# Optimization experiments

Measured on AMD Instinct MI355X. Metric: run time of the kernel, lower is better.

## Reference

```python
import jax, jax.numpy as jnp
import numpy as np

EPS = 1e-08


def setup_inputs() -> dict:
    key = jax.random.key(0)
    k1, k2 = jax.random.split(key)
    query_features = jax.random.normal(k1, (64, 1024, 32, 32), dtype=jnp.float32)
    support_features = jax.random.normal(k2, (25, 1024, 32, 32), dtype=jnp.float32)
    return {"query_features": query_features, "support_features": support_features}


def reference(query_features, support_features):
    B, C, h, w = support_features.shape
    NQ = query_features.shape[0]
    # Covariance over channels: flatten support to (C, B*h*w), center, GEMM.
    support = jnp.transpose(support_features, (1, 0, 2, 3)).reshape(C, -1)
    centered = support - jnp.mean(support, axis=1, keepdims=True)
    N = B * h * w
    cov = (centered @ centered.T) / (N - 1 + EPS)  # (C, C)
    # Queries: (NQ, C, d), L2-normalize each channel row over spatial dim.
    q = query_features.reshape(NQ, C, -1)
    q = q / (jnp.linalg.norm(q, axis=2, keepdims=True) + EPS)
    # diag(q^T cov q) without materializing (d, d): cov@q then elementwise reduce over C.
    cq = jnp.einsum('cD,nDd->ncd', cov, q)  # (NQ, C, d)
    scores = jnp.mean(jnp.sum(q * cq, axis=1), axis=1)  # (NQ,)
    return scores
```

## Files before the change

### kernel.cpp

```cpp
#include <hip/hip_runtime.h>

#define NQ   64
#define CCH  1024
#define DSP  1024
#define NSUP 25600
#define NKT  400
#define NCOVB 252

typedef __attribute__((ext_vector_type(4))) float f32x4;
typedef __attribute__((ext_vector_type(8))) __bf16 bf16x8;

#define WAITVM(N) asm volatile("s_waitcnt vmcnt(" #N ")" ::: "memory")
#define WAITLGKM0() asm volatile("s_waitcnt lgkmcnt(0)" ::: "memory")
#define BAR() __builtin_amdgcn_s_barrier()
#define SCHED0() __builtin_amdgcn_sched_barrier(0)

__device__ inline unsigned short f2bf(float x) {
  unsigned u = __builtin_bit_cast(unsigned, x);
  u += 0x7fffu + ((u >> 16) & 1u);
  return (unsigned short)(u >> 16);
}

__global__ __launch_bounds__(640) void mean_center_kernel(
    const float* __restrict__ sup, float* __restrict__ mean,
    unsigned short* __restrict__ Sb, int write_sb,
    float4* __restrict__ cov4, float4* __restrict__ out4) {
  __shared__ float wred[10];
  __shared__ float mbc;
  const int c = blockIdx.x;
  const int tid = threadIdx.x;
  const int l = tid & 63, wid = tid >> 6;
  const float4 z4 = make_float4(0.f, 0.f, 0.f, 0.f);
  if (tid < 256) cov4[c * 256 + tid] = z4;
  if (c == 0 && tid >= 256 && tid < 272) out4[tid - 256] = z4;

  float4 v[10];
  float s = 0.f;
#pragma unroll
  for (int i = 0; i < 10; ++i) {
    const int qd = i * 640 + tid;
    const int b = qd >> 8, s4 = (qd & 255) << 2;
    v[i] = *(const float4*)(sup + ((size_t)b * CCH + c) * DSP + s4);
    s += v[i].x + v[i].y + v[i].z + v[i].w;
  }
#pragma unroll
  for (int off = 32; off > 0; off >>= 1) s += __shfl_xor(s, off);
  if (l == 0) wred[wid] = s;
  __syncthreads();
  if (tid == 0) {
    float t = 0.f;
#pragma unroll
    for (int i = 0; i < 10; ++i) t += wred[i];
    mbc = t * (1.0f / 25600.0f);
  }
  __syncthreads();
  const float m = mbc;
  if (tid == 0) mean[c] = m;
  if (write_sb) {
#pragma unroll
    for (int i = 0; i < 10; ++i) {
      const int qd = i * 640 + tid;
      const int b = qd >> 8, s4 = (qd & 255) << 2;
      ushort4 o;
      o.x = f2bf(v[i].x - m); o.y = f2bf(v[i].y - m);
      o.z = f2bf(v[i].z - m); o.w = f2bf(v[i].w - m);
      *(ushort4*)(Sb + (size_t)c * NSUP + b * DSP + s4) = o;
    }
  }
}

__global__ __launch_bounds__(256) void qnorm_kernel(
    const float* __restrict__ q, float* __restrict__ qfac,
    unsigned short* __restrict__ Qb, int write_qb) {
  const int row = blockIdx.x * 4 + (threadIdx.x >> 6);
  const int l = threadIdx.x & 63;
  const float4* src = (const float4*)(q + (size_t)row * DSP);
  float4 v[4];
  float ss = 0.f;
#pragma unroll
  for (int i = 0; i < 4; ++i) {
    v[i] = src[l + 64 * i];
    ss += v[i].x * v[i].x + v[i].y * v[i].y + v[i].z * v[i].z + v[i].w * v[i].w;
  }
#pragma unroll
  for (int off = 32; off > 0; off >>= 1) ss += __shfl_xor(ss, off);
  const float f = 1.0f / (sqrtf(ss) + 1e-8f);
  if (l == 0) qfac[row] = f;
  if (write_qb) {
#pragma unroll
    for (int i = 0; i < 4; ++i) {
      ushort4 o;
      o.x = f2bf(v[i].x * f); o.y = f2bf(v[i].y * f);
      o.z = f2bf(v[i].z * f); o.w = f2bf(v[i].w * f);
      *(ushort4*)(Qb + (size_t)row * DSP + (size_t)(l + 64 * i) * 4) = o;
    }
  }
}


__device__ inline void rd4(const unsigned short* base, int r0, int col, int lr, bf16x8 f[4]) {
#pragma unroll
  for (int i = 0; i < 4; ++i)
    f[i] = *(const bf16x8*)(const void*)(base + (r0 + i * 16 + lr) * 64 + col);
}
__device__ inline void mfma16(const bf16x8 a[4], const bf16x8 b[4], f32x4 (*acc)[4]) {
#pragma unroll
  for (int i = 0; i < 4; ++i)
#pragma unroll
    for (int j = 0; j < 4; ++j)
      acc[i][j] = __builtin_amdgcn_mfma_f32_16x16x32_bf16(a[i], b[j], acc[i][j], 0, 0, 0);
}

__device__ inline void stage_glds(const unsigned short* __restrict__ src, int ld,
                                  int row0, int k0, unsigned short* lds) {
  const int tid = threadIdx.x;
  const int w = tid >> 6;
#pragma unroll
  for (int it = 0; it < 4; ++it) {
    const int ci = it * 256 + tid;
    const int r = ci >> 3;
    const int kc = ((ci & 7) ^ (r & 7)) << 3;
    const unsigned short* g = src + (size_t)(row0 + r) * ld + k0 + kc;
    unsigned short* lb = lds + ((it * 256 + w * 64) << 3);
    __builtin_amdgcn_global_load_lds((const __attribute__((address_space(1))) void*)g,
                                     (__attribute__((address_space(3))) void*)lb,
                                     16, 0, 0);
  }
}

__device__ inline void stage256g(const unsigned short* __restrict__ src, int ld,
                                 int row0, int k0, unsigned short* lds_base) {
  const int tid = threadIdx.x;
  const int wid = tid >> 6;
#pragma unroll
  for (int it = 0; it < 4; ++it) {
    const int ci = it * 512 + tid;
    const int r = ci >> 3;
    const int kc = ((ci & 7) ^ (r & 7)) << 3;
    const unsigned short* g = src + (size_t)(row0 + r) * ld + k0 + kc;
    unsigned short* lb = lds_base + ((it * 512 + (wid << 6)) << 3);
    __builtin_amdgcn_global_load_lds((const __attribute__((address_space(1))) void*)g,
                                     (__attribute__((address_space(3))) void*)lb,
                                     16, 0, 0);
  }
}

template <int NT>
__device__ inline void loop256(const unsigned short* __restrict__ src, int ld,
                               int rowA, int rowB, int k0, bool diag,
                               unsigned short* lds,
                               int wm, int wn, int lr, int kg, int sw,
                               f32x4 (*acc)[4]) {
  stage256g(src, ld, rowA, k0, lds);
  if (!diag) stage256g(src, ld, rowB, k0, lds + 16384);
  stage256g(src, ld, rowA, k0 + 64, lds + 32768);
  if (!diag) stage256g(src, ld, rowB, k0 + 64, lds + 32768 + 16384);

  for (int t = 0; t < NT; ++t) {
    const int cb = (t & 1) << 15;
    if (t < NT - 1) { if (diag) { WAITVM(4); } else { WAITVM(8); } }
    else { WAITVM(0); }
    BAR(); SCHED0();
    const unsigned short* A = lds + cb + wm * 8192;
    const unsigned short* B = lds + cb + (diag ? 0 : 16384) + (wn >> 1) * 8192;
    const int brow = (wn & 1) * 64;
    bf16x8 a[4], b[4];
    {
      const int col = kg ^ sw;
      rd4(B, brow, col, lr, b);
      rd4(A, 0, col, lr, a);
      mfma16(a, b, &acc[0]);
      rd4(A, 64, col, lr, a);
      mfma16(a, b, &acc[4]);
    }
    {
      const int col = (32 + kg) ^ sw;
      rd4(B, brow, col, lr, b);
      rd4(A, 0, col, lr, a);
      mfma16(a, b, &acc[0]);
      rd4(A, 64, col, lr, a);
      WAITLGKM0();
      BAR(); SCHED0();
      if (t + 2 < NT) {
        stage256g(src, ld, rowA, k0 + (t + 2) * 64, lds + cb);
        if (!diag) stage256g(src, ld, rowB, k0 + (t + 2) * 64, lds + cb + 16384);
      }
      mfma16(a, b, &acc[4]);
    }
  }
}

__device__ inline void decode_tile8(int t, int& ti, int& tj) {
  int rem = t; ti = 0;
  while (rem >= 8 - ti) { rem -= 8 - ti; ++ti; }
  tj = ti + rem;
}
__device__ inline void decode_pair4(int p, int& ti, int& tj) {
  int rem = p; ti = 0;
  while (rem >= 4 - ti) { rem -= 4 - ti; ++ti; }
  tj = ti + rem;
}

__global__ __launch_bounds__(256) void covq_kernel(
    const unsigned short* __restrict__ Sb, float* __restrict__ cov,
    const float* __restrict__ q, float* __restrict__ qfac,
    unsigned short* __restrict__ Qb) {
  __shared__ unsigned short clds[32768];
  const int bx = blockIdx.x;
  if (bx < NCOVB) {
    const int ks = bx % 7;
    int ti, tj; decode_tile8(bx / 7, ti, tj);
    const bool diag = (ti == tj);
    const int tid = threadIdx.x, l = tid & 63, w = tid >> 6;
    const int wr = (w >> 1) * 64, wc = (w & 1) * 64, lr = l & 15, kg = (l >> 4) * 8;
    const int sw = (lr & 7) << 3;
    f32x4 acc[4][4];
#pragma unroll
    for (int i = 0; i < 4; ++i)
#pragma unroll
      for (int j = 0; j < 4; ++j) acc[i][j] = 0.f;

    const int kt0 = (NKT * ks) / 7;
    const int nt = (NKT * (ks + 1)) / 7 - kt0;
    const int kbase = kt0 * 64;

    stage_glds(Sb, NSUP, ti * 128, kbase, clds);
    if (!diag) stage_glds(Sb, NSUP, tj * 128, kbase, clds + 8192);
    stage_glds(Sb, NSUP, ti * 128, kbase + 64, clds + 16384);
    if (!diag) stage_glds(Sb, NSUP, tj * 128, kbase + 64, clds + 16384 + 8192);
    for (int t = 0; t < nt; ++t) {
      const int cb = (t & 1) * 16384;
      if (t < nt - 1) { if (diag) { WAITVM(4); } else { WAITVM(8); } }
      else { WAITVM(0); }
      BAR(); SCHED0();
      const unsigned short* A = clds + cb;
      const unsigned short* B = diag ? A : A + 8192;
      const int col0 = kg ^ sw, col1 = (32 + kg) ^ sw;
      bf16x8 a[4], b[4];
      rd4(A, wr, col0, lr, a);
      rd4(B, wc, col0, lr, b);
      mfma16(a, b, (f32x4(*)[4])acc);
      rd4(A, wr, col1, lr, a);
      rd4(B, wc, col1, lr, b);
      WAITLGKM0();
      BAR(); SCHED0();
      if (t + 2 < nt) {
        const int k2 = kbase + (t + 2) * 64;
        stage_glds(Sb, NSUP, ti * 128, k2, clds + cb);
        if (!diag) stage_glds(Sb, NSUP, tj * 128, k2, clds + cb + 8192);
      }
      mfma16(a, b, (f32x4(*)[4])acc);
    }

    const float scale = 1.0f / (25599.0f + 1e-8f);
    const int rbase = ti * 128 + wr + (l >> 4) * 4;
    const int cbase = tj * 128 + wc + (l & 15);
#pragma unroll
    for (int i = 0; i < 4; ++i)
#pragma unroll
      for (int j = 0; j < 4; ++j)
#pragma unroll
        for (int r = 0; r < 4; ++r)
          atomicAdd(&cov[(size_t)(rbase + i * 16 + r) * CCH + cbase + j * 16],
                    acc[i][j][r] * scale);
  } else {
    const int row = (bx - NCOVB) * 4 + (threadIdx.x >> 6);
    const int l = threadIdx.x & 63;
    const float4* src = (const float4*)(q + (size_t)row * DSP);
    float4 v[4];
    float ss = 0.f;
#pragma unroll
    for (int i = 0; i < 4; ++i) {
      v[i] = src[l + 64 * i];
      ss += v[i].x * v[i].x + v[i].y * v[i].y + v[i].z * v[i].z + v[i].w * v[i].w;
    }
#pragma unroll
    for (int off = 32; off > 0; off >>= 1) ss += __shfl_xor(ss, off);
    const float f = 1.0f / (sqrtf(ss) + 1e-8f);
    if (l == 0) qfac[row] = f;
#pragma unroll
    for (int i = 0; i < 4; ++i) {
      ushort4 o;
      o.x = f2bf(v[i].x * f); o.y = f2bf(v[i].y * f);
      o.z = f2bf(v[i].z * f); o.w = f2bf(v[i].w * f);
      *(ushort4*)(Qb + (size_t)row * DSP + (size_t)(l + 64 * i) * 4) = o;
    }
  }
}

__global__ __launch_bounds__(512, 2) void gram256_kernel(
    const unsigned short* __restrict__ Qb, const float* __restrict__ cov,
    float* __restrict__ out) {
  __shared__ unsigned short lds[65536];
  const int wg = blockIdx.x;
  const int xcd = wg & 7, slot = wg >> 3;
  const int n = xcd * 8 + slot / 20;
  const int sub = slot % 20;
  const int kh = sub & 1;
  int ti, tj; decode_pair4(sub >> 1, ti, tj);
  const bool diag = (ti == tj);
  const int tid = threadIdx.x, l = tid & 63, wid = tid >> 6;
  const int wm = wid >> 2, wn = wid & 3;
  const int lr = l & 15, kg = (l >> 4) * 8;
  const int sw = (lr & 7) << 3;
  const unsigned short* Qn = Qb + (size_t)n * CCH * DSP;

  f32x4 acc[8][4];
#pragma unroll
  for (int i = 0; i < 8; ++i)
#pragma unroll
    for (int j = 0; j < 4; ++j) acc[i][j] = 0.f;

  loop256<8>(Qn, DSP, ti * 256, tj * 256, kh * 512, diag, lds,
             wm, wn, lr, kg, sw, acc);

  float wgt;
  if (!diag) wgt = 2.0f;
  else if (wm == 0 && (wn >> 1) == 1) wgt = 2.0f;
  else if (wm == 1 && (wn >> 1) == 0) wgt = 0.0f;
  else wgt = 1.0f;

  float s = 0.f;
  if (wgt != 0.0f) {
    const int rbase = ti * 256 + wm * 128 + (l >> 4) * 4;
    const int cbase = tj * 256 + wn * 64 + (l & 15);
#pragma unroll
    for (int i = 0; i < 8; ++i)
#pragma unroll
      for (int j = 0; j < 4; ++j)
#pragma unroll
        for (int r = 0; r < 4; ++r)
          s += acc[i][j][r] * cov[(size_t)(rbase + i * 16 + r) * CCH + cbase + j * 16];
  }
  s *= wgt * (1.0f / 1024.0f);
#pragma unroll
  for (int off = 32; off > 0; off >>= 1) s += __shfl_xor(s, off);
  if (l == 0) atomicAdd(&out[n], s);
}

__device__ inline void mfma16s(const bf16x8 a[4], const bf16x8 b[4], f32x4 acc[4][4]) {
#pragma unroll
  for (int i = 0; i < 4; ++i)
#pragma unroll
    for (int j = 0; j < 4; ++j)
      acc[i][j] = __builtin_amdgcn_mfma_f32_16x16x32_bf16(a[i], b[j], acc[i][j], 0, 0, 0);
}

__device__ inline void stage_sup_f32(const float* __restrict__ sup,
                                     const float* __restrict__ mean,
                                     int row0, int k0, unsigned short* lds) {
  const int tid = threadIdx.x;
#pragma unroll
  for (int it = 0; it < 4; ++it) {
    const int ci = it * 256 + tid;
    const int r = ci >> 3, kc = (ci & 7) << 3;
    const int c = row0 + r;
    const int k = k0 + kc;
    const int b = k >> 10, sp = k & 1023;
    const float4* gp = (const float4*)(sup + ((size_t)b * CCH + c) * DSP + sp);
    const float4 v0 = gp[0], v1 = gp[1];
    const float m = mean[c];
    union { unsigned short h[8]; int4 q; } pk;
    pk.h[0] = f2bf(v0.x - m); pk.h[1] = f2bf(v0.y - m);
    pk.h[2] = f2bf(v0.z - m); pk.h[3] = f2bf(v0.w - m);
    pk.h[4] = f2bf(v1.x - m); pk.h[5] = f2bf(v1.y - m);
    pk.h[6] = f2bf(v1.z - m); pk.h[7] = f2bf(v1.w - m);
    *(int4*)(lds + (size_t)(r * 8 + ((ci & 7) ^ (r & 7))) * 8) = pk.q;
  }
}
__device__ inline void stage_q_f32(const float* __restrict__ qn,
                                   const float* __restrict__ qfacn,
                                   int row0, int k0, unsigned short* lds) {
  const int tid = threadIdx.x;
#pragma unroll
  for (int it = 0; it < 4; ++it) {
    const int ci = it * 256 + tid;
    const int r = ci >> 3, kc = (ci & 7) << 3;
    const int c = row0 + r;
    const float4* gp = (const float4*)(qn + (size_t)c * DSP + k0 + kc);
    const float4 v0 = gp[0], v1 = gp[1];
    const float f = qfacn[c];
    union { unsigned short h[8]; int4 q; } pk;
    pk.h[0] = f2bf(v0.x * f); pk.h[1] = f2bf(v0.y * f);
    pk.h[2] = f2bf(v0.z * f); pk.h[3] = f2bf(v0.w * f);
    pk.h[4] = f2bf(v1.x * f); pk.h[5] = f2bf(v1.y * f);
    pk.h[6] = f2bf(v1.z * f); pk.h[7] = f2bf(v1.w * f);
    *(int4*)(lds + (size_t)(r * 8 + ((ci & 7) ^ (r & 7))) * 8) = pk.q;
  }
}
__device__ inline void compute_step(const unsigned short* lA, const unsigned short* lB,
                                    int wr, int wc, int lr, int kg, f32x4 acc[4][4]) {
  const int sc = (lr & 7) << 3;
#pragma unroll
  for (int kk = 0; kk < 64; kk += 32) {
    const int col = (kk + kg) ^ sc;
    bf16x8 a[4], b[4];
    rd4(lA, wr, col, lr, a);
    rd4(lB, wc, col, lr, b);
    mfma16s(a, b, acc);
  }
}

__global__ __launch_bounds__(256) void cov_kernel_f32(
    const float* __restrict__ sup, const float* __restrict__ mean,
    float* __restrict__ cov) {
  __shared__ unsigned short clds[32768];
  const int wg = blockIdx.x;
  const int ks = wg & 7;
  int ti, tj; decode_tile8(wg >> 3, ti, tj);
  const bool diag = (ti == tj);
  const int tid = threadIdx.x, l = tid & 63, w = tid >> 6;
  const int wr = (w >> 1) * 64, wc = (w & 1) * 64, lr = l & 15, kg = (l >> 4) * 8;
  f32x4 acc[4][4];
#pragma unroll
  for (int i = 0; i < 4; ++i)
#pragma unroll
    for (int j = 0; j < 4; ++j) acc[i][j] = 0.f;

  const int kbase = ks * (NSUP / 8);
  stage_sup_f32(sup, mean, ti * 128, kbase, clds);
  if (!diag) stage_sup_f32(sup, mean, tj * 128, kbase, clds + 8192);
  __syncthreads();
  for (int kt = 0; kt < 50; ++kt) {
    const int cb = (kt & 1) * 16384;
    const int nb = cb ^ 16384;
    if (kt + 1 < 50) {
      const int k1 = kbase + (kt + 1) * 64;
      stage_sup_f32(sup, mean, ti * 128, k1, clds + nb);
      if (!diag) stage_sup_f32(sup, mean, tj * 128, k1, clds + nb + 8192);
    }
    compute_step(clds + cb, diag ? clds + cb : clds + cb + 8192, wr, wc, lr, kg, acc);
    __syncthreads();
  }
  const float scale = 1.0f / (25599.0f + 1e-8f);
  const int rbase = ti * 128 + wr + (l >> 4) * 4;
  const int cbase = tj * 128 + wc + (l & 15);
#pragma unroll
  for (int i = 0; i < 4; ++i)
#pragma unroll
    for (int j = 0; j < 4; ++j)
#pragma unroll
      for (int r = 0; r < 4; ++r)
        atomicAdd(&cov[(size_t)(rbase + i * 16 + r) * CCH + cbase + j * 16],
                  acc[i][j][r] * scale);
}

__global__ __launch_bounds__(256) void gram_kernel_f32(
    const float* __restrict__ q, const float* __restrict__ qfac,
    const float* __restrict__ cov, float* __restrict__ out) {
  __shared__ unsigned short lA[2][128 * 64];
  __shared__ unsigned short lB[2][128 * 64];
  const int wg = blockIdx.x;
  const int xcd = wg & 7, slot = wg >> 3;
  const int n = xcd * 8 + slot / 36;
  int ti, tj; decode_tile8(slot % 36, ti, tj);
  const bool diag = (ti == tj);
  const int tid = threadIdx.x, l = tid & 63, w = tid >> 6;
  const int wr = (w >> 1) * 64, wc = (w & 1) * 64, lr = l & 15, kg = (l >> 4) * 8;
  f32x4 acc[4][4];
#pragma unroll
  for (int i = 0; i < 4; ++i)
#pragma unroll
    for (int j = 0; j < 4; ++j) acc[i][j] = 0.f;

  const float* qn = q + (size_t)n * CCH * DSP;
  const float* qfacn = qfac + (size_t)n * CCH;

  stage_q_f32(qn, qfacn, ti * 128, 0, lA[0]);
  if (!diag) stage_q_f32(qn, qfacn, tj * 128, 0, lB[0]);
  __syncthreads();
  int cur = 0;
  for (int kt = 0; kt < 16; ++kt) {
    if (kt + 1 < 16) {
      const int k1 = (kt + 1) * 64;
      stage_q_f32(qn, qfacn, ti * 128, k1, lA[cur ^ 1]);
      if (!diag) stage_q_f32(qn, qfacn, tj * 128, k1, lB[cur ^ 1]);
    }
    compute_step(lA[cur], diag ? lA[cur] : lB[cur], wr, wc, lr, kg, acc);
    __syncthreads();
    cur ^= 1;
  }

  float s = 0.f;
  const int rbase = ti * 128 + wr + (l >> 4) * 4;
  const int cbase = tj * 128 + wc + (l & 15);
#pragma unroll
  for (int i = 0; i < 4; ++i)
#pragma unroll
    for (int j = 0; j < 4; ++j)
#pragma unroll
      for (int r = 0; r < 4; ++r)
        s += acc[i][j][r] * cov[(size_t)(rbase + i * 16 + r) * CCH + cbase + j * 16];
  if (!diag) s *= 2.0f;
  s *= (1.0f / 1024.0f);
#pragma unroll
  for (int off = 32; off > 0; off >>= 1) s += __shfl_xor(s, off);
  if (l == 0) atomicAdd(&out[n], s);
}

extern "C" void kernel_launch(void* const* d_in, const int* in_sizes, int n_in,
                              void* d_out, int out_size, void* d_ws, size_t ws_size,
                              hipStream_t stream) {
  const float* q = (const float*)d_in[0];
  const float* sup = (const float*)d_in[1];
  float* out = (float*)d_out;

  char* ws = (char*)d_ws;
  float* mean = (float*)ws;
  float* qfac = (float*)(ws + (4 << 10));
  float* cov  = (float*)(ws + (4 << 10) + (256 << 10));
  unsigned short* Sb = (unsigned short*)(ws + (4 << 10) + (256 << 10) + (4 << 20));
  unsigned short* Qb = Sb + (size_t)CCH * NSUP;
  const size_t need_fat = (size_t)(4 << 10) + (256 << 10) + (4 << 20) +
                          (size_t)CCH * NSUP * 2 + (size_t)NQ * CCH * DSP * 2;
  const bool fat = ws_size >= need_fat;

  mean_center_kernel<<<CCH, 640, 0, stream>>>(sup, mean, Sb, fat ? 1 : 0,
                                              (float4*)cov, (float4*)out);

  if (fat) {
    covq_kernel<<<dim3(NCOVB + NQ * CCH / 4), 256, 0, stream>>>(Sb, cov, q, qfac, Qb);
    gram256_kernel<<<dim3(1280), 512, 0, stream>>>(Qb, cov, out);
  } else {
    qnorm_kernel<<<NQ * CCH / 4, 256, 0, stream>>>(q, qfac, (unsigned short*)0, 0);
    cov_kernel_f32<<<dim3(288), 256, 0, stream>>>(sup, mean, cov);
    gram_kernel_f32<<<dim3(8 * 8 * 36), 256, 0, stream>>>(q, qfac, cov, out);
  }
}
```

Measured before the change: 254.0 us.

## Replace 256-tile pipelined gram kernel with simpler 128-tile single-buffered kernel

Swaps the 256x256-tile, double-buffered, split-K gram kernel (512 threads, 1280 blocks) for a 128x128-tile kernel with 256 threads and 2304 blocks. The new kernel covers the full K range in each block, loads global data straight into LDS with one buffer, and synchronises twice per k-step. This removes the split-K work and the complex diagonal weighting. In exchange it lowers data reuse per tile and drops the overlap between loads and compute, so the kernel may stall more on memory.

```diff
diff --git a/kernel.cpp b/kernel.cpp
--- a/kernel.cpp
+++ b/kernel.cpp
@@ -128,76 +128,9 @@
   }
 }
 
-__device__ inline void stage256g(const unsigned short* __restrict__ src, int ld,
-                                 int row0, int k0, unsigned short* lds_base) {
-  const int tid = threadIdx.x;
-  const int wid = tid >> 6;
-#pragma unroll
-  for (int it = 0; it < 4; ++it) {
-    const int ci = it * 512 + tid;
-    const int r = ci >> 3;
-    const int kc = ((ci & 7) ^ (r & 7)) << 3;
-    const unsigned short* g = src + (size_t)(row0 + r) * ld + k0 + kc;
-    unsigned short* lb = lds_base + ((it * 512 + (wid << 6)) << 3);
-    __builtin_amdgcn_global_load_lds((const __attribute__((address_space(1))) void*)g,
-                                     (__attribute__((address_space(3))) void*)lb,
-                                     16, 0, 0);
-  }
-}
-
-template <int NT>
-__device__ inline void loop256(const unsigned short* __restrict__ src, int ld,
-                               int rowA, int rowB, int k0, bool diag,
-                               unsigned short* lds,
-                               int wm, int wn, int lr, int kg, int sw,
-                               f32x4 (*acc)[4]) {
-  stage256g(src, ld, rowA, k0, lds);
-  if (!diag) stage256g(src, ld, rowB, k0, lds + 16384);
-  stage256g(src, ld, rowA, k0 + 64, lds + 32768);
-  if (!diag) stage256g(src, ld, rowB, k0 + 64, lds + 32768 + 16384);
-
-  for (int t = 0; t < NT; ++t) {
-    const int cb = (t & 1) << 15;
-    if (t < NT - 1) { if (diag) { WAITVM(4); } else { WAITVM(8); } }
-    else { WAITVM(0); }
-    BAR(); SCHED0();
-    const unsigned short* A = lds + cb + wm * 8192;
-    const unsigned short* B = lds + cb + (diag ? 0 : 16384) + (wn >> 1) * 8192;
-    const int brow = (wn & 1) * 64;
-    bf16x8 a[4], b[4];
-    {
-      const int col = kg ^ sw;
-      rd4(B, brow, col, lr, b);
-      rd4(A, 0, col, lr, a);
-      mfma16(a, b, &acc[0]);
-      rd4(A, 64, col, lr, a);
-      mfma16(a, b, &acc[4]);
-    }
-    {
-      const int col = (32 + kg) ^ sw;
-      rd4(B, brow, col, lr, b);
-      rd4(A, 0, col, lr, a);
-      mfma16(a, b, &acc[0]);
-      rd4(A, 64, col, lr, a);
-      WAITLGKM0();
-      BAR(); SCHED0();
-      if (t + 2 < NT) {
-        stage256g(src, ld, rowA, k0 + (t + 2) * 64, lds + cb);
-        if (!diag) stage256g(src, ld, rowB, k0 + (t + 2) * 64, lds + cb + 16384);
-      }
-      mfma16(a, b, &acc[4]);
-    }
-  }
-}
-
 __device__ inline void decode_tile8(int t, int& ti, int& tj) {
   int rem = t; ti = 0;
   while (rem >= 8 - ti) { rem -= 8 - ti; ++ti; }
-  tj = ti + rem;
-}
-__device__ inline void decode_pair4(int p, int& ti, int& tj) {
-  int rem = p; ti = 0;
-  while (rem >= 4 - ti) { rem -= 4 - ti; ++ti; }
   tj = ti + rem;
 }
 
@@ -288,51 +221,55 @@
   }
 }
 
-__global__ __launch_bounds__(512, 2) void gram256_kernel(
+__global__ __launch_bounds__(256) void gram128_kernel(
     const unsigned short* __restrict__ Qb, const float* __restrict__ cov,
     float* __restrict__ out) {
-  __shared__ unsigned short lds[65536];
+  __shared__ unsigned short lA[8192];
+  __shared__ unsigned short lB[8192];
   const int wg = blockIdx.x;
   const int xcd = wg & 7, slot = wg >> 3;
-  const int n = xcd * 8 + slot / 20;
-  const int sub = slot % 20;
-  const int kh = sub & 1;
-  int ti, tj; decode_pair4(sub >> 1, ti, tj);
+  const int n = xcd * 8 + slot / 36;
+  int ti, tj; decode_tile8(slot % 36, ti, tj);
   const bool diag = (ti == tj);
-  const int tid = threadIdx.x, l = tid & 63, wid = tid >> 6;
-  const int wm = wid >> 2, wn = wid & 3;
-  const int lr = l & 15, kg = (l >> 4) * 8;
+  const int tid = threadIdx.x, l = tid & 63, w = tid >> 6;
+  const int wr = (w >> 1) * 64, wc = (w & 1) * 64, lr = l & 15, kg = (l >> 4) * 8;
   const int sw = (lr & 7) << 3;
   const unsigned short* Qn = Qb + (size_t)n * CCH * DSP;
 
-  f32x4 acc[8][4];
-#pragma unroll
-  for (int i = 0; i < 8; ++i)
+  f32x4 acc[4][4];
+#pragma unroll
+  for (int i = 0; i < 4; ++i)
 #pragma unroll
     for (int j = 0; j < 4; ++j) acc[i][j] = 0.f;
 
-  loop256<8>(Qn, DSP, ti * 256, tj * 256, kh * 512, diag, lds,
-             wm, wn, lr, kg, sw, acc);
-
-  float wgt;
-  if (!diag) wgt = 2.0f;
-  else if (wm == 0 && (wn >> 1) == 1) wgt = 2.0f;
-  else if (wm == 1 && (wn >> 1) == 0) wgt = 0.0f;
-  else wgt = 1.0f;
+  for (int kt = 0; kt < 16; ++kt) {
+    stage_glds(Qn, DSP, ti * 128, kt * 64, lA);
+    if (!diag) stage_glds(Qn, DSP, tj * 128, kt * 64, lB);
+    __syncthreads();
+    const unsigned short* B = diag ? lA : lB;
+    const int col0 = kg ^ sw, col1 = (32 + kg) ^ sw;
+    bf16x8 a[4], b[4];
+    rd4(lA, wr, col0, lr, a);
+    rd4(B, wc, col0, lr, b);
+    mfma16(a, b, (f32x4(*)[4])acc);
+    rd4(lA, wr, col1, lr, a);
+    rd4(B, wc, col1, lr, b);
+    mfma16(a, b, (f32x4(*)[4])acc);
+    __syncthreads();
+  }
 
   float s = 0.f;
-  if (wgt != 0.0f) {
-    const int rbase = ti * 256 + wm * 128 + (l >> 4) * 4;
-    const int cbase = tj * 256 + wn * 64 + (l & 15);
-#pragma unroll
-    for (int i = 0; i < 8; ++i)
-#pragma unroll
-      for (int j = 0; j < 4; ++j)
-#pragma unroll
-        for (int r = 0; r < 4; ++r)
-          s += acc[i][j][r] * cov[(size_t)(rbase + i * 16 + r) * CCH + cbase + j * 16];
-  }
-  s *= wgt * (1.0f / 1024.0f);
+  const int rbase = ti * 128 + wr + (l >> 4) * 4;
+  const int cbase = tj * 128 + wc + (l & 15);
+#pragma unroll
+  for (int i = 0; i < 4; ++i)
+#pragma unroll
+    for (int j = 0; j < 4; ++j)
+#pragma unroll
+      for (int r = 0; r < 4; ++r)
+        s += acc[i][j][r] * cov[(size_t)(rbase + i * 16 + r) * CCH + cbase + j * 16];
+  if (!diag) s *= 2.0f;
+  s *= (1.0f / 1024.0f);
 #pragma unroll
   for (int off = 32; off > 0; off >>= 1) s += __shfl_xor(s, off);
   if (l == 0) atomicAdd(&out[n], s);
@@ -520,7 +457,7 @@
 
   if (fat) {
     covq_kernel<<<dim3(NCOVB + NQ * CCH / 4), 256, 0, stream>>>(Sb, cov, q, qfac, Qb);
-    gram256_kernel<<<dim3(1280), 512, 0, stream>>>(Qb, cov, out);
+    gram128_kernel<<<dim3(2304), 256, 0, stream>>>(Qb, cov, out);
   } else {
     qnorm_kernel<<<NQ * CCH / 4, 256, 0, stream>>>(q, qfac, (unsigned short*)0, 0);
     cov_kernel_f32<<<dim3(288), 256, 0, stream>>>(sup, mean, cov);
```

After: 270.5 us. 6.5% more time.
